# Optimization experiments

Hardware: AMD Instinct MI355X
Metric: run time of the kernel (lower is better)

## Reference

```python
import jax, jax.numpy as jnp
import numpy as np

N_NODES = 20000
IN_CH = 512
HEADS = 8
CH = 64  # hidden_layer per head
E = 320000
E_LABEL = 100000


def setup_inputs() -> dict:
    key = jax.random.key(0)
    ks = jax.random.split(key, 8)
    x = jax.random.normal(ks[0], (N_NODES, IN_CH), dtype=jnp.float32)
    edge_index = jax.random.randint(ks[1], (2, E), 0, N_NODES)
    edge_label_index = jax.random.randint(ks[2], (2, E_LABEL), 0, N_NODES)
    # GATv2Conv params (share_weights=False, bias=True)
    sc = 1.0 / np.sqrt(IN_CH)
    W_l = jax.random.normal(ks[3], (IN_CH, HEADS * CH), dtype=jnp.float32) * sc
    W_r = jax.random.normal(ks[4], (IN_CH, HEADS * CH), dtype=jnp.float32) * sc
    att = jax.random.normal(ks[5], (HEADS, CH), dtype=jnp.float32) * (1.0 / np.sqrt(CH))
    bias = jnp.zeros((HEADS * CH,), dtype=jnp.float32)
    gamma = jnp.ones((HEADS * CH,), dtype=jnp.float32)
    beta = jnp.zeros((HEADS * CH,), dtype=jnp.float32)
    return {"x": x, "edge_index": edge_index, "edge_label_index": edge_label_index,
            "W_l": W_l, "W_r": W_r, "att": att, "bias": bias,
            "gamma": gamma, "beta": beta}


def reference(x, edge_index, edge_label_index, W_l, W_r, att, bias, gamma, beta):
    N = x.shape[0]
    H, C = att.shape
    src, dst = edge_index[0], edge_index[1]
    # GATv2Conv: separate source/target linear maps
    xl = (x @ W_l).reshape(N, H, C)
    xr = (x @ W_r).reshape(N, H, C)
    # per-edge attention logits (GATv2: leaky_relu BEFORE attention vector)
    e = jax.nn.leaky_relu(xl[src] + xr[dst], negative_slope=0.2)  # [E,H,C]
    alpha = jnp.einsum('ehc,hc->eh', e, att)                      # [E,H]
    # softmax over incoming edges of each destination node
    amax = jax.ops.segment_max(alpha, dst, num_segments=N)        # [N,H]
    alpha = jnp.exp(alpha - amax[dst])
    denom = jax.ops.segment_sum(alpha, dst, num_segments=N)       # [N,H]
    alpha = alpha / (denom[dst] + 1e-16)
    # scatter-add aggregation of attended source messages
    out = jax.ops.segment_sum(alpha[:, :, None] * xl[src], dst, num_segments=N)  # [N,H,C]
    out = out.reshape(N, H * C) + bias
    # BatchNorm1d (training-mode batch stats, eps=1e-5)
    mu = out.mean(axis=0)
    var = out.var(axis=0)
    out = (out - mu) * jax.lax.rsqrt(var + 1e-5) * gamma + beta
    out = jax.nn.relu(out)  # dropout is identity in deterministic reference
    # gather + dot-product link scoring
    s = out[edge_label_index[0]]
    t = out[edge_label_index[1]]
    return jnp.sum(s * t, axis=1)  # [E_LABEL]
```

## Files before the change

kernel.cpp:

```cpp
#include <hip/hip_runtime.h>
#include <hip/hip_bf16.h>
#include <cstdint>

#define IN_CH 512
#define HC    512
#define HEADS 8
#define NPACK 1024

typedef __attribute__((ext_vector_type(8))) short bf16x8;
typedef __attribute__((ext_vector_type(8))) ushort u16x8;
typedef __attribute__((ext_vector_type(4))) float f32x4;
typedef __attribute__((ext_vector_type(2))) float f32x2;
typedef const __attribute__((address_space(1))) uint8_t* gaddr_t;
typedef __attribute__((address_space(3))) uint8_t* laddr_t;

__device__ inline ushort f2bf(float f) {
  uint32_t u = __float_as_uint(f);
  return (ushort)((u + 0x7fffu + ((u >> 16) & 1u)) >> 16);
}
__device__ inline float bf2f(ushort u) {
  return __uint_as_float(((uint32_t)u) << 16);
}

#if defined(__has_builtin)
#if __has_builtin(__builtin_amdgcn_cvt_pk_f32_fp8) && __has_builtin(__builtin_amdgcn_cvt_pk_fp8_f32)
#define HAVE_HW_FP8 1
#endif
#endif

__device__ __forceinline__ float fp8_decode_sw(uint32_t v) {
  const uint32_t t = v & 0x7fu;
  float m;
  if (t >= 8u) m = __uint_as_float((((t >> 3) + 120u) << 23) | ((t & 7u) << 20));
  else m = (float)t * 0.001953125f;
  return (v & 0x80u) ? -m : m;
}
__device__ __forceinline__ uint8_t fp8_encode_sw(float f) {
  const uint32_t b = __float_as_uint(f);
  const uint32_t s = (b >> 24) & 0x80u;
  uint32_t a = b & 0x7fffffffu;
  if (a >= 0x43e00000u) return (uint8_t)(s | 0x7eu);
  if (a < 0x3c800000u) {
    const int qi = (int)(__uint_as_float(a) * 512.0f + 0.5f);
    return (uint8_t)(s | (qi >= 8 ? 8u : (uint32_t)qi));
  }
  const uint32_t r = a + 0x7ffffu + ((a >> 20) & 1u);
  const uint32_t e = r >> 23;
  if (e > 135u) return (uint8_t)(s | 0x7eu);
  return (uint8_t)(s | ((e - 120u) << 3) | ((r >> 20) & 7u));
}

__device__ __forceinline__ void fp8x2_to_f32(uint32_t u, float& f0, float& f1, bool hi) {
#ifdef HAVE_HW_FP8
  const f32x2 p = hi ? __builtin_amdgcn_cvt_pk_f32_fp8(u, true)
                     : __builtin_amdgcn_cvt_pk_f32_fp8(u, false);
  f0 = p.x; f1 = p.y;
#else
  const uint32_t w = hi ? (u >> 16) : u;
  f0 = fp8_decode_sw(w & 0xffu);
  f1 = fp8_decode_sw((w >> 8) & 0xffu);
#endif
}
__device__ __forceinline__ uint8_t f32_to_fp8(float f) {
#ifdef HAVE_HW_FP8
  return (uint8_t)(__builtin_amdgcn_cvt_pk_fp8_f32(f, f, 0, false) & 0xff);
#else
  return fp8_encode_sw(f);
#endif
}

template<int CTRL>
__device__ __forceinline__ float dpp_add(float s) {
  const int t = __builtin_amdgcn_update_dpp(0, __float_as_int(s), CTRL, 0xf, 0xf, true);
  return s + __int_as_float(t);
}

__global__ void prep(const float* __restrict__ x, ushort* __restrict__ xb,
                     const float* __restrict__ Wl, const float* __restrict__ Wr,
                     ushort* __restrict__ bt,
                     const int* __restrict__ ei, int* __restrict__ counts,
                     const int* __restrict__ eli, int* __restrict__ counts2,
                     int n4, int E, int EL, int nbc, int nbp, int nbh) {
  const int b = blockIdx.x;
  if (b < nbc) {
    const int i = b * 256 + threadIdx.x;
    if (i < n4) {
      const float4 v = ((const float4*)x)[i];
      ushort4 o;
      o.x = f2bf(v.x); o.y = f2bf(v.y); o.z = f2bf(v.z); o.w = f2bf(v.w);
      ((ushort4*)xb)[i] = o;
    }
  } else if (b < nbc + nbp) {
    const int i = (b - nbc) * 256 + threadIdx.x;
    if (i < NPACK * IN_CH) {
      const int n = i >> 9, k = i & 511;
      const float v = (n < HC) ? Wl[(size_t)k * HC + n] : Wr[(size_t)k * HC + (n - HC)];
      bt[i] = f2bf(v);
    }
  } else if (b < nbc + nbp + nbh) {
    const int e = (b - nbc - nbp) * 256 + threadIdx.x;
    if (e < E) atomicAdd(&counts[ei[E + e]], 1);
  } else {
    const int e = (b - nbc - nbp - nbh) * 256 + threadIdx.x;
    if (e < EL) atomicAdd(&counts2[eli[e]], 1);
  }
}

__global__ __launch_bounds__(512) void gemm_mfma(
    const ushort* __restrict__ xb, const ushort* __restrict__ bt,
    uint8_t* __restrict__ xl8, ushort* __restrict__ xrb, int M) {
  __shared__ __align__(16) ushort As[3][256 * 32];
  __shared__ __align__(16) ushort Bs[3][128 * 32];
  const int sw  = (blockIdx.x & 7) * 79 + (blockIdx.x >> 3);
  const int row0 = (sw >> 3) * 256;
  const int col0 = (sw & 7) * 128;
  const int wave = threadIdx.x >> 6, lane = threadIdx.x & 63;
  const int quad = lane >> 4, m16 = lane & 15;
  const int wrow = (wave >> 1) * 64;
  const int wcol = (wave & 1) * 64;
  const int srow = lane >> 2;
  const int scol = (lane & 3) * 8;
  const f32x4 zero = {0.f, 0.f, 0.f, 0.f};
  f32x4 acc[4][4];
  #pragma unroll
  for (int i = 0; i < 4; ++i)
    #pragma unroll
    for (int j = 0; j < 4; ++j) acc[i][j] = zero;

  auto stage = [&](int buf, int kt) {
    const int k0 = kt * 32;
    const int r = wave * 16 + srow;
    const ushort* ga0 = xb + (size_t)(row0 + r) * IN_CH + k0 + scol;
    __builtin_amdgcn_global_load_lds((gaddr_t)ga0, (laddr_t)(&As[buf][(wave * 16) * 32]), 16, 0, 0);
    const ushort* ga1 = xb + (size_t)(row0 + 128 + r) * IN_CH + k0 + scol;
    __builtin_amdgcn_global_load_lds((gaddr_t)ga1, (laddr_t)(&As[buf][(128 + wave * 16) * 32]), 16, 0, 0);
    const ushort* gb = bt + (size_t)(col0 + r) * IN_CH + k0 + scol;
    __builtin_amdgcn_global_load_lds((gaddr_t)gb, (laddr_t)(&Bs[buf][(wave * 16) * 32]), 16, 0, 0);
  };
  auto compute = [&](int buf) {
    bf16x8 af[4], bfr[4];
    #pragma unroll
    for (int i = 0; i < 4; ++i)
      af[i] = *(const bf16x8*)(&As[buf][(wrow + i * 16 + m16) * 32 + quad * 8]);
    #pragma unroll
    for (int j = 0; j < 4; ++j)
      bfr[j] = *(const bf16x8*)(&Bs[buf][(wcol + j * 16 + m16) * 32 + quad * 8]);
    #pragma unroll
    for (int i = 0; i < 4; ++i)
      #pragma unroll
      for (int j = 0; j < 4; ++j)
        acc[i][j] = __builtin_amdgcn_mfma_f32_16x16x32_bf16(af[i], bfr[j], acc[i][j], 0, 0, 0);
  };

  stage(0, 0);
  stage(1, 1);
  int buf = 0;
  for (int kt = 0; kt <= 13; ++kt) {
    asm volatile("s_waitcnt vmcnt(3)" ::: "memory");
    __builtin_amdgcn_s_barrier();
    int nbuf = buf + 2; if (nbuf >= 3) nbuf -= 3;
    stage(nbuf, kt + 2);
    compute(buf);
    ++buf; if (buf == 3) buf = 0;
  }
  asm volatile("s_waitcnt vmcnt(3)" ::: "memory");
  __builtin_amdgcn_s_barrier();
  compute(buf);
  ++buf; if (buf == 3) buf = 0;
  asm volatile("s_waitcnt vmcnt(0)" ::: "memory");
  __builtin_amdgcn_s_barrier();
  compute(buf);

  const bool isL = (col0 < HC);
  if (isL) {
    #pragma unroll
    for (int i = 0; i < 4; ++i) {
      const int r = row0 + wrow + i * 16 + quad * 4;
      #pragma unroll
      for (int j = 0; j < 4; ++j) {
        const int cg = col0 + wcol + j * 16 + m16;
        #pragma unroll
        for (int t = 0; t < 4; ++t) {
          const int rr = r + t;
          if (rr < M) xl8[(size_t)rr * HC + cg] = f32_to_fp8(acc[i][j][t]);
        }
      }
    }
  } else {
    const int cbase = col0 - HC;
    #pragma unroll
    for (int i = 0; i < 4; ++i) {
      const int r = row0 + wrow + i * 16 + quad * 4;
      #pragma unroll
      for (int j = 0; j < 4; ++j) {
        const int cg = cbase + wcol + j * 16 + m16;
        #pragma unroll
        for (int t = 0; t < 4; ++t) {
          const int rr = r + t;
          if (rr < M) xrb[(size_t)rr * HC + cg] = f2bf(acc[i][j][t]);
        }
      }
    }
  }
}

__global__ __launch_bounds__(256) void scan_fused(
    const int* __restrict__ cA, int* __restrict__ oA, int* __restrict__ curA,
    int* __restrict__ fA,
    const int* __restrict__ cB, int* __restrict__ oB, int* __restrict__ curB,
    int* __restrict__ fB, int Nn, int nb) {
  const int half = (blockIdx.x >= nb) ? 1 : 0;
  const int blk  = blockIdx.x - half * nb;
  const int* counts = half ? cB : cA;
  int* offsets = half ? oB : oA;
  int* cursor  = half ? curB : curA;
  int* flags   = half ? fB : fA;
  __shared__ int tmp[256];
  __shared__ int sPref;
  const int t = threadIdx.x;
  const int i = blk * 256 + t;
  const int v = (i < Nn) ? counts[i] : 0;
  tmp[t] = v;
  __syncthreads();
  for (int d = 1; d < 256; d <<= 1) {
    int add = (t >= d) ? tmp[t - d] : 0;
    __syncthreads();
    tmp[t] += add;
    __syncthreads();
  }
  if (t == 0) atomicExch(&flags[blk], tmp[255] + 1);
  if (t < 64) {
    int s = 0;
    for (int b = t; b < blk; b += 64) {
      int f;
      do { f = atomicOr(&flags[b], 0); } while (f == 0);
      s += f - 1;
    }
    #pragma unroll
    for (int off = 32; off > 0; off >>= 1) s += __shfl_down(s, off, 64);
    if (t == 0) sPref = s;
  }
  __syncthreads();
  const int pref = sPref;
  if (i < Nn) {
    const int o = tmp[t] - v + pref;
    offsets[i] = o;
    cursor[i] = o;
  }
}

__global__ void csr_fill(const int* __restrict__ ei, int* __restrict__ cursor,
                         int* __restrict__ csr_src,
                         const int* __restrict__ eli, int* __restrict__ cursor2,
                         int* __restrict__ csr_t, int* __restrict__ csr_eid,
                         int E, int EL, int nbE) {
  const int b = blockIdx.x;
  if (b < nbE) {
    const int e = b * 256 + threadIdx.x;
    if (e < E) {
      const int pos = atomicAdd(&cursor[ei[E + e]], 1);
      csr_src[pos] = ei[e];
    }
  } else {
    const int e = (b - nbE) * 256 + threadIdx.x;
    if (e < EL) {
      const int pos = atomicAdd(&cursor2[eli[e]], 1);
      csr_t[pos] = eli[EL + e];
      csr_eid[pos] = e;
    }
  }
}

__global__ __launch_bounds__(256) void gatv2_agg(
    const uint8_t* __restrict__ xl8, const ushort* xrb, const float* __restrict__ att,
    const int* __restrict__ offsets, const int* __restrict__ counts,
    const int* __restrict__ csr_src, ushort* agg, int Nn) {
  const int node = blockIdx.x * 4 + (threadIdx.x >> 6);
  const int lane = threadIdx.x & 63;
  if (node >= Nn) return;
  const int start = offsets[node];
  const int deg   = counts[node];
  float rv[8], tv[8];
  {
    const u16x8 ur = *(const u16x8*)(xrb + (size_t)node * HC + lane * 8);
    #pragma unroll
    for (int c = 0; c < 8; ++c) rv[c] = bf2f((ushort)ur[c]);
    const float4* pa = (const float4*)(att + lane * 8);
    const float4 t0 = pa[0], t1 = pa[1];
    tv[0]=t0.x; tv[1]=t0.y; tv[2]=t0.z; tv[3]=t0.w;
    tv[4]=t1.x; tv[5]=t1.y; tv[6]=t1.z; tv[7]=t1.w;
  }
  float acc[8] = {};
  float densum = 0.f;
  const int* ps = csr_src + start;
  auto row = [&](int idx) {
    return *(const uint2*)(xl8 + (size_t)ps[idx] * HC + lane * 8);
  };
  auto body = [&](const uint2 cur) {
    float a[8];
    fp8x2_to_f32(cur.x, a[0], a[1], false);
    fp8x2_to_f32(cur.x, a[2], a[3], true);
    fp8x2_to_f32(cur.y, a[4], a[5], false);
    fp8x2_to_f32(cur.y, a[6], a[7], true);
    float s0 = 0.f, s1 = 0.f;
    #pragma unroll
    for (int c = 0; c < 4; ++c) {
      const float v = a[c] + rv[c];
      s0 += fmaxf(v, 0.2f * v) * tv[c];
    }
    #pragma unroll
    for (int c = 4; c < 8; ++c) {
      const float v = a[c] + rv[c];
      s1 += fmaxf(v, 0.2f * v) * tv[c];
    }
    float s = s0 + s1;
    s = dpp_add<0xB1>(s);
    s = dpp_add<0x4E>(s);
    s = dpp_add<0x141>(s);
    const float ea = __expf(s);
    densum += ea;
    #pragma unroll
    for (int c = 0; c < 8; ++c) acc[c] += ea * a[c];
  };

  uint2 b0 = {}, b1 = {};
  if (deg > 0) b0 = row(0);
  if (deg > 1) b1 = row(1);
  int i = 0;
  for (; i + 2 <= deg; i += 2) {
    const uint2 c0 = b0;
    if (i + 2 < deg) b0 = row(i + 2);
    const uint2 c1 = b1;
    if (i + 3 < deg) b1 = row(i + 3);
    body(c0);
    body(c1);
  }
  if (i < deg) body(b0);

  const float inv = 1.0f / (densum + 1e-16f);
  ushort* pd = agg + (size_t)node * HC + lane * 8;
  ushort4 o0, o1;
  o0.x = f2bf(acc[0] * inv); o0.y = f2bf(acc[1] * inv);
  o0.z = f2bf(acc[2] * inv); o0.w = f2bf(acc[3] * inv);
  o1.x = f2bf(acc[4] * inv); o1.y = f2bf(acc[5] * inv);
  o1.z = f2bf(acc[6] * inv); o1.w = f2bf(acc[7] * inv);
  *(ushort4*)(pd + 0) = o0;
  *(ushort4*)(pd + 4) = o1;
}

__global__ void bn_stats(const ushort* __restrict__ agg, float* __restrict__ gsum,
                         float* __restrict__ gsq, int* __restrict__ ctr,
                         const float* __restrict__ gamma, const float* __restrict__ beta,
                         float* __restrict__ aScale, float* __restrict__ bShift,
                         float invN, int Nn) {
  const int t = threadIdx.x;
  const int rows_per_block = (Nn + gridDim.x - 1) / gridDim.x;
  const int r0 = blockIdx.x * rows_per_block;
  const int r1 = min(Nn, r0 + rows_per_block);
  float s0 = 0.f, s1 = 0.f, q0 = 0.f, q1 = 0.f;
  for (int r = r0; r < r1; ++r) {
    const ushort2 u = ((const ushort2*)(agg + (size_t)r * HC))[t];
    const float v0 = bf2f(u.x), v1 = bf2f(u.y);
    s0 += v0; q0 += v0 * v0;
    s1 += v1; q1 += v1 * v1;
  }
  atomicAdd(&gsum[2 * t], s0);
  atomicAdd(&gsum[2 * t + 1], s1);
  atomicAdd(&gsq[2 * t], q0);
  atomicAdd(&gsq[2 * t + 1], q1);
  __shared__ int isLast;
  __syncthreads();
  if (t == 0) {
    __threadfence();
    isLast = (atomicAdd(ctr, 1) == (int)gridDim.x - 1) ? 1 : 0;
  }
  __syncthreads();
  if (isLast) {
    #pragma unroll
    for (int k = 0; k < 2; ++k) {
      const int c = t + k * 256;
      const float sum = atomicAdd(&gsum[c], 0.0f);
      const float sq  = atomicAdd(&gsq[c], 0.0f);
      const float m = sum * invN;
      const float var = sq * invN - m * m;
      const float rs = rsqrtf(var + 1e-5f);
      const float a = rs * gamma[c];
      aScale[c] = a;
      bShift[c] = beta[c] - m * a;
    }
  }
}

__global__ __launch_bounds__(256) void score_g(
    const ushort* __restrict__ agg, const float* __restrict__ aScale,
    const float* __restrict__ bShift, const int* __restrict__ off2,
    const int* __restrict__ cnt2, const int* __restrict__ csr_t,
    const int* __restrict__ csr_eid, float* __restrict__ out, int Nn) {
  const int node = blockIdx.x * 4 + (threadIdx.x >> 6);
  const int lane = threadIdx.x & 63;
  if (node >= Nn) return;
  const int start = off2[node];
  const int deg   = cnt2[node];
  if (deg == 0) return;
  float aS[8], bS[8], ys[8];
  {
    const float4* pa = (const float4*)(aScale + lane * 8);
    const float4 a0 = pa[0], a1 = pa[1];
    aS[0]=a0.x; aS[1]=a0.y; aS[2]=a0.z; aS[3]=a0.w;
    aS[4]=a1.x; aS[5]=a1.y; aS[6]=a1.z; aS[7]=a1.w;
    const float4* pb = (const float4*)(bShift + lane * 8);
    const float4 c0 = pb[0], c1 = pb[1];
    bS[0]=c0.x; bS[1]=c0.y; bS[2]=c0.z; bS[3]=c0.w;
    bS[4]=c1.x; bS[5]=c1.y; bS[6]=c1.z; bS[7]=c1.w;
    const u16x8 us = *(const u16x8*)(agg + (size_t)node * HC + lane * 8);
    #pragma unroll
    for (int c = 0; c < 8; ++c)
      ys[c] = fmaxf(0.f, bf2f((ushort)us[c]) * aS[c] + bS[c]);
  }
  const int* pt = csr_t + start;
  const int* pe = csr_eid + start;
  auto row = [&](int idx) {
    return *(const u16x8*)(agg + (size_t)pt[idx] * HC + lane * 8);
  };
  auto emit = [&](const u16x8 ut, int eid) {
    float s0 = 0.f, s1 = 0.f;
    #pragma unroll
    for (int c = 0; c < 4; ++c)
      s0 += ys[c] * fmaxf(0.f, bf2f((ushort)ut[c]) * aS[c] + bS[c]);
    #pragma unroll
    for (int c = 4; c < 8; ++c)
      s1 += ys[c] * fmaxf(0.f, bf2f((ushort)ut[c]) * aS[c] + bS[c]);
    float s = s0 + s1;
    s = dpp_add<0xB1>(s);
    s = dpp_add<0x4E>(s);
    s = dpp_add<0x141>(s);
    s = dpp_add<0x140>(s);
    s = dpp_add<0x142>(s);
    s = dpp_add<0x143>(s);
    if (lane == 63) out[eid] = s;
  };
  u16x8 b0 = {}, b1 = {};
  b0 = row(0);
  if (deg > 1) b1 = row(1);
  int j = 0;
  for (; j + 2 <= deg; j += 2) {
    const u16x8 c0 = b0;
    if (j + 2 < deg) b0 = row(j + 2);
    const u16x8 c1 = b1;
    if (j + 3 < deg) b1 = row(j + 3);
    emit(c0, pe[j]);
    emit(c1, pe[j + 1]);
  }
  if (j < deg) emit(b0, pe[j]);
}

extern "C" void kernel_launch(void* const* d_in, const int* in_sizes, int n_in,
                              void* d_out, int out_size, void* d_ws, size_t ws_size,
                              hipStream_t stream) {
  const float* x     = (const float*)d_in[0];
  const int*   ei    = (const int*)d_in[1];
  const int*   eli   = (const int*)d_in[2];
  const float* W_l   = (const float*)d_in[3];
  const float* W_r   = (const float*)d_in[4];
  const float* att   = (const float*)d_in[5];
  const float* gamma = (const float*)d_in[7];
  const float* beta  = (const float*)d_in[8];
  float* out = (float*)d_out;

  const int Nn = in_sizes[0] / IN_CH;
  const int E  = in_sizes[1] / 2;
  const int EL = in_sizes[2] / 2;

  uint8_t* xl8 = (uint8_t*)d_ws;
  ushort* xrb = (ushort*)d_ws + (size_t)Nn * HC;
  ushort* xbf = xrb + (size_t)Nn * HC;
  ushort* btb = xbf + (size_t)Nn * IN_CH;
  int* counts   = (int*)(btb + (size_t)NPACK * IN_CH);
  int* counts2  = counts + Nn;
  float* gsum   = (float*)(counts2 + Nn);
  float* gsq    = gsum + HC;
  int* flagsA   = (int*)(gsq + HC);
  int* flagsB   = flagsA + 128;
  int* bnctr    = flagsB + 128;
  int* offsets  = bnctr + 64;
  int* cursor   = offsets + Nn;
  int* offsets2 = cursor + Nn;
  int* cursor2  = offsets2 + Nn;
  int* csr_src  = cursor2 + Nn;
  int* csr_t    = csr_src + E;
  int* csr_eid  = csr_t + EL;
  float* aScale = (float*)(csr_eid + EL);
  float* bShift = aScale + HC;
  ushort* agg = xrb;

  const int nb  = (Nn + 255) / 256;
  const int nbc = (Nn * IN_CH / 4 + 255) / 256;
  const int nbp = (NPACK * IN_CH + 255) / 256;
  const int nbh = (E + 255) / 256;
  const int nbh2 = (EL + 255) / 256;

  (void)hipMemsetAsync(counts, 0, (2 * (size_t)Nn + 2 * HC + 320) * sizeof(int), stream);

  prep<<<nbc + nbp + nbh + nbh2, 256, 0, stream>>>(
      x, xbf, W_l, W_r, btb, ei, counts, eli, counts2,
      Nn * IN_CH / 4, E, EL, nbc, nbp, nbh);

  gemm_mfma<<<632, 512, 0, stream>>>(xbf, btb, xl8, xrb, Nn);

  scan_fused<<<2 * nb, 256, 0, stream>>>(counts, offsets, cursor, flagsA,
                                         counts2, offsets2, cursor2, flagsB, Nn, nb);
  csr_fill<<<nbh + nbh2, 256, 0, stream>>>(ei, cursor, csr_src,
                                           eli, cursor2, csr_t, csr_eid, E, EL, nbh);

  gatv2_agg<<<(Nn + 3) / 4, 256, 0, stream>>>(xl8, xrb, att, offsets, counts,
                                              csr_src, agg, Nn);

  bn_stats<<<200, 256, 0, stream>>>(agg, gsum, gsq, bnctr, gamma, beta,
                                    aScale, bShift, 1.0f / (float)Nn, Nn);

  score_g<<<(Nn + 3) / 4, 256, 0, stream>>>(agg, aScale, bShift, offsets2,
                                            counts2, csr_t, csr_eid, out, Nn);
}
```

Measured before the change: 277.4 us.

## Fuse scan and CSR fill via grid barrier; pack label CSR as int2

Merges the prefix-scan kernel and the CSR fill kernel into one launch, using a global atomic counter as a grid-wide barrier after the offsets are written. The merged kernel then fills CSR with a grid-stride loop over only 2*nb blocks. It also packs the label target and edge id into a single int2 array so score_g does one load per edge instead of two. This saves a launch and its gap, but the spin barrier requires all blocks to be co-resident, and the fill step now runs with far fewer threads.

```diff
diff --git a/kernel.cpp b/kernel.cpp
--- a/kernel.cpp
+++ b/kernel.cpp
@@ -204,11 +204,14 @@
   }
 }
 
-__global__ __launch_bounds__(256) void scan_fused(
+__global__ __launch_bounds__(256) void scan_fill(
     const int* __restrict__ cA, int* __restrict__ oA, int* __restrict__ curA,
     int* __restrict__ fA,
     const int* __restrict__ cB, int* __restrict__ oB, int* __restrict__ curB,
-    int* __restrict__ fB, int Nn, int nb) {
+    int* __restrict__ fB,
+    const int* __restrict__ ei, int* __restrict__ csr_src,
+    const int* __restrict__ eli, int2* __restrict__ csr_te,
+    int* __restrict__ doneCtr, int Nn, int nb, int E, int EL) {
   const int half = (blockIdx.x >= nb) ? 1 : 0;
   const int blk  = blockIdx.x - half * nb;
   const int* counts = half ? cB : cA;
@@ -241,33 +244,27 @@
     if (t == 0) sPref = s;
   }
   __syncthreads();
-  const int pref = sPref;
   if (i < Nn) {
-    const int o = tmp[t] - v + pref;
+    const int o = tmp[t] - v + sPref;
     offsets[i] = o;
     cursor[i] = o;
   }
-}
-
-__global__ void csr_fill(const int* __restrict__ ei, int* __restrict__ cursor,
-                         int* __restrict__ csr_src,
-                         const int* __restrict__ eli, int* __restrict__ cursor2,
-                         int* __restrict__ csr_t, int* __restrict__ csr_eid,
-                         int E, int EL, int nbE) {
-  const int b = blockIdx.x;
-  if (b < nbE) {
-    const int e = b * 256 + threadIdx.x;
-    if (e < E) {
-      const int pos = atomicAdd(&cursor[ei[E + e]], 1);
-      csr_src[pos] = ei[e];
-    }
-  } else {
-    const int e = (b - nbE) * 256 + threadIdx.x;
-    if (e < EL) {
-      const int pos = atomicAdd(&cursor2[eli[e]], 1);
-      csr_t[pos] = eli[EL + e];
-      csr_eid[pos] = e;
-    }
+  __threadfence();
+  __syncthreads();
+  if (t == 0) {
+    atomicAdd(doneCtr, 1);
+    while (atomicOr(doneCtr, 0) < 2 * nb) {}
+  }
+  __syncthreads();
+  const int gid = blockIdx.x * 256 + t;
+  const int stride = gridDim.x * 256;
+  for (int e = gid; e < E; e += stride) {
+    const int pos = atomicAdd(&curA[ei[E + e]], 1);
+    csr_src[pos] = ei[e];
+  }
+  for (int e = gid; e < EL; e += stride) {
+    const int pos = atomicAdd(&curB[eli[e]], 1);
+    csr_te[pos] = make_int2(eli[EL + e], e);
   }
 }
 
@@ -394,8 +391,8 @@
 __global__ __launch_bounds__(256) void score_g(
     const ushort* __restrict__ agg, const float* __restrict__ aScale,
     const float* __restrict__ bShift, const int* __restrict__ off2,
-    const int* __restrict__ cnt2, const int* __restrict__ csr_t,
-    const int* __restrict__ csr_eid, float* __restrict__ out, int Nn) {
+    const int* __restrict__ cnt2, const int2* __restrict__ csr_te,
+    float* __restrict__ out, int Nn) {
   const int node = blockIdx.x * 4 + (threadIdx.x >> 6);
   const int lane = threadIdx.x & 63;
   if (node >= Nn) return;
@@ -417,10 +414,9 @@
     for (int c = 0; c < 8; ++c)
       ys[c] = fmaxf(0.f, bf2f((ushort)us[c]) * aS[c] + bS[c]);
   }
-  const int* pt = csr_t + start;
-  const int* pe = csr_eid + start;
+  const int2* pte = csr_te + start;
   auto row = [&](int idx) {
-    return *(const u16x8*)(agg + (size_t)pt[idx] * HC + lane * 8);
+    return *(const u16x8*)(agg + (size_t)pte[idx].x * HC + lane * 8);
   };
   auto emit = [&](const u16x8 ut, int eid) {
     float s0 = 0.f, s1 = 0.f;
@@ -448,10 +444,10 @@
     if (j + 2 < deg) b0 = row(j + 2);
     const u16x8 c1 = b1;
     if (j + 3 < deg) b1 = row(j + 3);
-    emit(c0, pe[j]);
-    emit(c1, pe[j + 1]);
-  }
-  if (j < deg) emit(b0, pe[j]);
+    emit(c0, pte[j].y);
+    emit(c1, pte[j + 1].y);
+  }
+  if (j < deg) emit(b0, pte[j].y);
 }
 
 extern "C" void kernel_launch(void* const* d_in, const int* in_sizes, int n_in,
@@ -482,14 +478,14 @@
   int* flagsA   = (int*)(gsq + HC);
   int* flagsB   = flagsA + 128;
   int* bnctr    = flagsB + 128;
+  int* doneCtr  = bnctr + 32;
   int* offsets  = bnctr + 64;
   int* cursor   = offsets + Nn;
   int* offsets2 = cursor + Nn;
   int* cursor2  = offsets2 + Nn;
   int* csr_src  = cursor2 + Nn;
-  int* csr_t    = csr_src + E;
-  int* csr_eid  = csr_t + EL;
-  float* aScale = (float*)(csr_eid + EL);
+  int2* csr_te  = (int2*)(csr_src + E);
+  float* aScale = (float*)(csr_te + EL);
   float* bShift = aScale + HC;
   ushort* agg = xrb;
 
@@ -507,10 +503,10 @@
 
   gemm_mfma<<<632, 512, 0, stream>>>(xbf, btb, xl8, xrb, Nn);
 
-  scan_fused<<<2 * nb, 256, 0, stream>>>(counts, offsets, cursor, flagsA,
-                                         counts2, offsets2, cursor2, flagsB, Nn, nb);
-  csr_fill<<<nbh + nbh2, 256, 0, stream>>>(ei, cursor, csr_src,
-                                           eli, cursor2, csr_t, csr_eid, E, EL, nbh);
+  scan_fill<<<2 * nb, 256, 0, stream>>>(counts, offsets, cursor, flagsA,
+                                        counts2, offsets2, cursor2, flagsB,
+                                        ei, csr_src, eli, csr_te,
+                                        doneCtr, Nn, nb, E, EL);
 
   gatv2_agg<<<(Nn + 3) / 4, 256, 0, stream>>>(xl8, xrb, att, offsets, counts,
                                               csr_src, agg, Nn);
@@ -519,5 +515,5 @@
                                     aScale, bShift, 1.0f / (float)Nn, Nn);
 
   score_g<<<(Nn + 3) / 4, 256, 0, stream>>>(agg, aScale, bShift, offsets2,
-                                            counts2, csr_t, csr_eid, out, Nn);
-}
+                                            counts2, csr_te, out, Nn);
+}
```

After: 290.5 us. +4.7%, slower.
